# Kernel tuning notes

Hardware: AMD Instinct MI355X
Metric: run time of the kernel (lower is better)

Reference implementation:

```python
import jax, jax.numpy as jnp
import numpy as np

N, E, C, A, R = 8192, 65536, 64, 16, 8
DIMS = (1, 3, 5, 7)        # dims of l = 0..3 irrep blocks
IRDIM = sum(DIMS)          # 16
L = len(DIMS)              # 4 TP paths (0e x l -> l, 'uvu')
WN = L * C                 # conv_tp weight_numel = 256
HID = 64                   # radial MLP hidden width
AVG_NUM_NEIGH = 16.0


def setup_inputs() -> dict:
    key = jax.random.key(0)
    ks = jax.random.split(key, 18)
    f = lambda k, s: jax.random.normal(k, s, dtype=jnp.float32)
    return dict(
        node_attrs=f(ks[0], (N, A)),
        node_feats=f(ks[1], (N, C)),
        edge_attrs=f(ks[2], (E, IRDIM)),
        edge_feats=f(ks[3], (E, R)),
        edge_index=jax.random.randint(ks[4], (2, E), 0, N),
        magmom_node_inv_feats=f(ks[5], (N, R)),
        magmom_node_attrs=f(ks[6], (N, IRDIM)),
        # learned parameters (e3nn-style, no biases, 1/sqrt(fan_in) path norm)
        W_up=f(ks[7], (C, C)),
        W_r0=f(ks[8], (R + R, HID)),
        W_r1=f(ks[9], (HID, HID)),
        W_r2=f(ks[10], (HID, HID)),
        W_r3=f(ks[11], (HID, WN)),
        W_trans=f(ks[12], (WN, WN)),
        W_dens=f(ks[13], (R, 1)),
        W_lin=f(ks[14], (L, C, C)),
        W_mlin=f(ks[15], (L, C, C)),
        W_skip=f(ks[16], (L, C, A, C)),
        W_mskip=f(ks[17], (L, C, A, C)),
    )


def _per_l_linear(x, W):
    # equivariant Linear: independent channel-mixing per l block. x: [N,C,16]
    outs, o = [], 0
    for l, d in enumerate(DIMS):
        outs.append(jnp.einsum('ncm,cd->ndm', x[:, :, o:o + d], W[l]) / np.sqrt(C))
        o += d
    return jnp.concatenate(outs, axis=-1)


def _skip_tp(x, attrs, W):
    # FullyConnectedTensorProduct with scalar (0e) node attrs: (l x 0e -> l, 'uvw')
    outs, o = [], 0
    for l, d in enumerate(DIMS):
        outs.append(jnp.einsum('num,nv,uvw->nwm', x[:, :, o:o + d], attrs, W[l]) / np.sqrt(C * A))
        o += d
    return jnp.concatenate(outs, axis=-1)


def _weighted_tp(xj, attrs_e, w):
    # weighted TP of 0e node feats with lmax=3 attrs: per-edge 'uvu' weights.
    # xj: [E,C], attrs_e: [E,16], w: [E,L,C] -> [E,C,16]
    wf = jnp.repeat(w, np.array(DIMS), axis=1, total_repeat_length=IRDIM)  # [E,16,C]
    return xj[:, :, None] * attrs_e[:, None, :] * jnp.swapaxes(wf, 1, 2)


def reference(node_attrs, node_feats, edge_attrs, edge_feats, edge_index,
              magmom_node_inv_feats, magmom_node_attrs,
              W_up, W_r0, W_r1, W_r2, W_r3, W_trans, W_dens,
              W_lin, W_mlin, W_skip, W_mskip):
    sender, receiver = edge_index[0], edge_index[1]
    x = node_feats @ W_up / np.sqrt(C)                     # linear_up (0e)
    xj = x[sender]                                         # gather by sender
    h = jnp.concatenate([edge_feats, magmom_node_inv_feats[sender]], axis=-1)
    for W in (W_r0, W_r1, W_r2):                           # radial MLP (silu)
        h = jax.nn.silu(h @ W / np.sqrt(W.shape[0]))
    tp_w = (h @ W_r3 / np.sqrt(HID)).reshape(E, L, C)      # per-edge TP weights
    edge_density = jnp.tanh((edge_feats @ W_dens / np.sqrt(R)) ** 2)  # [E,1]
    mji = _weighted_tp(xj, edge_attrs, tp_w)               # [E,C,16]
    tp_w_m = (tp_w.reshape(E, WN) @ W_trans / np.sqrt(WN)).reshape(E, L, C)
    magmom_mji = _weighted_tp(xj, magmom_node_attrs[sender], tp_w_m)
    density = jax.ops.segment_sum(edge_density, receiver, num_segments=N)       # [N,1]
    message = jax.ops.segment_sum(mji, receiver, num_segments=N)                # [N,C,16]
    magmom_message = jax.ops.segment_sum(magmom_mji, receiver, num_segments=N)
    message = _per_l_linear(message, W_lin) / (density[:, :, None] + 1.0)
    message = _skip_tp(message, node_attrs, W_skip)
    magmom_message = _per_l_linear(magmom_message, W_mlin) / AVG_NUM_NEIGH
    magmom_message = _skip_tp(magmom_message, node_attrs, W_mskip)
    return message, magmom_message                         # each [N,C,16] (reshape_irreps layout)
```

## Files before the change

### kernel.cpp

```cpp
#include <hip/hip_runtime.h>

#define N_NODES 8192
#define N_EDGES 65536

typedef __attribute__((ext_vector_type(8))) short bf16x8;
typedef __attribute__((ext_vector_type(4))) float f32x4;

static __device__ __forceinline__ float bfl(unsigned v){ unsigned u=v<<16; float f; __builtin_memcpy(&f,&u,4); return f; }
static __device__ __forceinline__ float bfh(unsigned v){ unsigned u=v&0xffff0000u; float f; __builtin_memcpy(&f,&u,4); return f; }
static __device__ __forceinline__ float bfs(unsigned short h){ unsigned u=((unsigned)h)<<16; float f; __builtin_memcpy(&f,&u,4); return f; }
static __device__ __forceinline__ unsigned short f2bf(float f){ unsigned u; __builtin_memcpy(&u,&f,4); u += 0x7fffu + ((u>>16)&1u); return (unsigned short)(u>>16); }
static __device__ __forceinline__ unsigned pk(float a, float b){ return (unsigned)f2bf(a) | ((unsigned)f2bf(b)<<16); }
static __device__ __forceinline__ float silu_f(float v){ return v/(1.f+__expf(-v)); }

__global__ __launch_bounds__(256) void k_linup(const float* __restrict__ nf,
                                               const float* __restrict__ wup,
                                               float* __restrict__ x){
    __shared__ float s[4][64];
    const int t=threadIdx.x, wv=t>>6, lane=t&63;
    const int n=blockIdx.x*4+wv;
    s[wv][lane]=nf[(size_t)n*64+lane];
    __syncthreads();
    float acc=0.f;
    for(int c=0;c<64;++c) acc += s[wv][c]*wup[c*64+lane];
    x[(size_t)n*64+lane]=acc*0.125f;
}

__global__ __launch_bounds__(256) void k_wmlp(const float* __restrict__ wr0,
                                              const float* __restrict__ wr1,
                                              const float* __restrict__ wr2,
                                              unsigned short* __restrict__ w0f,
                                              unsigned short* __restrict__ w1f,
                                              unsigned short* __restrict__ w2f){
    const int b=blockIdx.x, t=threadIdx.x;
    #pragma unroll
    for(int z=0;z<2;++z){
        int idx=t*2+z;
        int lane=idx>>3, i=idx&7;
        if(b<4){
            int nt=b, k=(lane>>4)*8+i, n=nt*16+(lane&15);
            float v=(k<16)? wr0[k*64+n]*0.25f : 0.f;
            w0f[(nt*64+lane)*8+i]=f2bf(v);
        } else if(b<12){
            int q=b-4, nt=q>>1, ks=q&1;
            int k=ks*32+(lane>>4)*8+i, n=nt*16+(lane&15);
            w1f[((nt*2+ks)*64+lane)*8+i]=f2bf(wr1[k*64+n]*0.125f);
        } else {
            int q=b-12, nt=q>>1, ks=q&1;
            int k=ks*32+(lane>>4)*8+i, n=nt*16+(lane&15);
            w2f[((nt*2+ks)*64+lane)*8+i]=f2bf(wr2[k*64+n]*0.125f);
        }
    }
}

__global__ __launch_bounds__(256) void k_w3t(const float* __restrict__ wr3,
                                             const float* __restrict__ wtr,
                                             float* __restrict__ wt){
    const int k=blockIdx.x, n=threadIdx.x;
    float acc=0.f;
    for(int kk=0;kk<256;++kk) acc += wr3[k*256+kk]*wtr[kk*256+n];
    wt[k*256+n]=acc;
}

__global__ __launch_bounds__(256) void k_wtf(const float* __restrict__ wr3,
                                             const float* __restrict__ wt,
                                             unsigned short* __restrict__ wtf){
    const int b=blockIdx.x;
    const int mt=b>>1, ks=b&1, t=threadIdx.x;
    #pragma unroll
    for(int z=0;z<2;++z){
        int idx=t*2+z;
        int lane=idx>>3, i=idx&7;
        int k=ks*32+(lane>>4)*8+i;
        int n=mt*16+(lane&15);
        int j=n>>3, s=n&7;
        float v = (s<4)? wr3[k*256+s*64+j]*0.125f
                       : wt[k*256+(s-4)*64+j]*(1.f/128.f);
        wtf[((size_t)b*64+lane)*8+i]=f2bf(v);
    }
}

__global__ __launch_bounds__(256) void k_wwf(const float* __restrict__ wlin,
                                             const float* __restrict__ wmlin,
                                             const float* __restrict__ wskip,
                                             const float* __restrict__ wmskip,
                                             unsigned* __restrict__ wwf){
    const int b=blockIdx.x, ten=b>>8, lc=b&255, l=lc>>6, c=lc&63;
    const float* WL = ten? wmlin:wlin;
    const float* WS = ten? wmskip:wskip;
    const float scale = ten? (1.f/4096.f):(1.f/256.f);
    const int t=threadIdx.x, wg=t>>6, s=t&63, lane=s>>1, half=s&1;
    const int kg=lane>>4, w=wg*16+(lane&15);
    const int v0=kg*8+half*4;
    float a0=0,a1=0,a2=0,a3=0;
    for(int u=0;u<64;++u){
        float wl=WL[(l*64+c)*64+u];
        const float* wsp=&WS[(((l*64+u)*16+v0)*64)+w];
        a0+=wl*wsp[0]; a1+=wl*wsp[64]; a2+=wl*wsp[128]; a3+=wl*wsp[192];
    }
    size_t fi=(((size_t)ten*4+l)*64+c)*4+wg;
    unsigned* op=wwf + (fi*32+lane)*4 + half*2;
    op[0]=pk(a0*scale,a1*scale); op[1]=pk(a2*scale,a3*scale);
}

__global__ __launch_bounds__(256) void k_count(const int* __restrict__ recv, int* __restrict__ cnt){
    int e=blockIdx.x*256+threadIdx.x;
    atomicAdd(&cnt[recv[e]],1);
}
__global__ __launch_bounds__(1024) void k_scan(const int* __restrict__ cnt, int* __restrict__ rowptr, int* __restrict__ cur){
    __shared__ int s[1024];
    const int t=threadIdx.x;
    int c[8]; int sum=0;
    #pragma unroll
    for(int i=0;i<8;++i){ c[i]=cnt[t*8+i]; sum+=c[i]; }
    s[t]=sum; __syncthreads();
    for(int off=1;off<1024;off<<=1){
        int v=s[t]; int add=(t>=off)? s[t-off]:0;
        __syncthreads();
        s[t]=v+add;
        __syncthreads();
    }
    int run=s[t]-sum;
    #pragma unroll
    for(int i=0;i<8;++i){ rowptr[t*8+i]=run; cur[t*8+i]=run; run+=c[i]; }
    if(t==1023) rowptr[8192]=run;
}
__global__ __launch_bounds__(256) void k_scatter(const int* __restrict__ recv, int* __restrict__ cur, int* __restrict__ elist){
    int e=blockIdx.x*256+threadIdx.x;
    int r=recv[e];
    int p=atomicAdd(&cur[r],1);
    elist[p]=e;
}

__global__ __launch_bounds__(256) void k_edge2(
    const float* __restrict__ ef, const float* __restrict__ mminv,
    const int* __restrict__ sender,
    const float* __restrict__ wdens,
    const uint4* __restrict__ w0f, const uint4* __restrict__ w1f,
    const uint4* __restrict__ w2f, const uint4* __restrict__ wtf,
    const float* __restrict__ x,
    unsigned short* __restrict__ wxc, float* __restrict__ ed)
{
    __shared__ unsigned short hA[4096];
    __shared__ unsigned short hB[4096];
    __shared__ float xs[64*68];
    const int t=threadIdx.x, lane=t&63, wv=t>>6;
    const int tile=blockIdx.x*64;

    {
        const int e=t>>2, q=t&3, ge=tile+e;
        const int s=sender[ge];
        const float4* xp=(const float4*)(x+(size_t)s*64+q*16);
        float4* xw=(float4*)&xs[e*68+q*16];
        xw[0]=xp[0]; xw[1]=xp[1]; xw[2]=xp[2]; xw[3]=xp[3];
        const int se3=(e&7)<<3;
        if(q==0){
            float4 f0=*(const float4*)(ef+(size_t)ge*8);
            float4 f1=*(const float4*)(ef+(size_t)ge*8+4);
            uint4 o; o.x=pk(f0.x,f0.y); o.y=pk(f0.z,f0.w); o.z=pk(f1.x,f1.y); o.w=pk(f1.z,f1.w);
            *(uint4*)&hA[e*64 + (0^se3)]=o;
            float acc=f0.x*wdens[0]+f0.y*wdens[1]+f0.z*wdens[2]+f0.w*wdens[3]
                     +f1.x*wdens[4]+f1.y*wdens[5]+f1.z*wdens[6]+f1.w*wdens[7];
            acc*=0.35355339059327373f;
            float q2=acc*acc;
            float ex=__expf(2.f*q2);
            ed[ge]=1.f-2.f/(ex+1.f);
        } else if(q==1){
            float4 f0=*(const float4*)(mminv+(size_t)s*8);
            float4 f1=*(const float4*)(mminv+(size_t)s*8+4);
            uint4 o; o.x=pk(f0.x,f0.y); o.y=pk(f0.z,f0.w); o.z=pk(f1.x,f1.y); o.w=pk(f1.z,f1.w);
            *(uint4*)&hA[e*64 + (8^se3)]=o;
        } else if(q==2){
            *(uint4*)&hA[e*64 + (16^se3)]=make_uint4(0,0,0,0);
        } else {
            *(uint4*)&hA[e*64 + (24^se3)]=make_uint4(0,0,0,0);
        }
    }
    __syncthreads();

    const int arow=wv*16+(lane&15);
    const int akg=lane>>4;
    const int aswz=(arow&7)<<3;
    const int dcol=lane&15;
    const int drow0=wv*16+(lane>>4)*4;

    {
        uint4 av=*(const uint4*)&hA[arow*64+((akg*8)^aswz)];
        bf16x8 a; __builtin_memcpy(&a,&av,16);
        f32x4 d[4];
        #pragma unroll
        for(int nt=0;nt<4;++nt){
            uint4 bw=w0f[nt*64+lane];
            bf16x8 b; __builtin_memcpy(&b,&bw,16);
            f32x4 z={0.f,0.f,0.f,0.f};
            d[nt]=__builtin_amdgcn_mfma_f32_16x16x32_bf16(a,b,z,0,0,0);
        }
        #pragma unroll
        for(int nt=0;nt<4;++nt){
            #pragma unroll
            for(int r=0;r<4;++r){
                int e2=drow0+r, n=nt*16+dcol;
                hB[e2*64 + (n^((e2&7)<<3))]=f2bf(silu_f(d[nt][r]));
            }
        }
    }
    __syncthreads();

    {
        uint4 av0=*(const uint4*)&hB[arow*64+(((0+akg)*8)^aswz)];
        uint4 av1=*(const uint4*)&hB[arow*64+(((4+akg)*8)^aswz)];
        bf16x8 a0,a1; __builtin_memcpy(&a0,&av0,16); __builtin_memcpy(&a1,&av1,16);
        f32x4 d[4];
        #pragma unroll
        for(int nt=0;nt<4;++nt){
            uint4 bw0=w1f[(nt*2+0)*64+lane];
            uint4 bw1=w1f[(nt*2+1)*64+lane];
            bf16x8 b0,b1; __builtin_memcpy(&b0,&bw0,16); __builtin_memcpy(&b1,&bw1,16);
            f32x4 z={0.f,0.f,0.f,0.f};
            d[nt]=__builtin_amdgcn_mfma_f32_16x16x32_bf16(a0,b0,z,0,0,0);
            d[nt]=__builtin_amdgcn_mfma_f32_16x16x32_bf16(a1,b1,d[nt],0,0,0);
        }
        #pragma unroll
        for(int nt=0;nt<4;++nt){
            #pragma unroll
            for(int r=0;r<4;++r){
                int e2=drow0+r, n=nt*16+dcol;
                hA[e2*64 + (n^((e2&7)<<3))]=f2bf(silu_f(d[nt][r]));
            }
        }
    }
    __syncthreads();

    {
        uint4 av0=*(const uint4*)&hA[arow*64+(((0+akg)*8)^aswz)];
        uint4 av1=*(const uint4*)&hA[arow*64+(((4+akg)*8)^aswz)];
        bf16x8 a0,a1; __builtin_memcpy(&a0,&av0,16); __builtin_memcpy(&a1,&av1,16);
        f32x4 d[4];
        #pragma unroll
        for(int nt=0;nt<4;++nt){
            uint4 bw0=w2f[(nt*2+0)*64+lane];
            uint4 bw1=w2f[(nt*2+1)*64+lane];
            bf16x8 b0,b1; __builtin_memcpy(&b0,&bw0,16); __builtin_memcpy(&b1,&bw1,16);
            f32x4 z={0.f,0.f,0.f,0.f};
            d[nt]=__builtin_amdgcn_mfma_f32_16x16x32_bf16(a0,b0,z,0,0,0);
            d[nt]=__builtin_amdgcn_mfma_f32_16x16x32_bf16(a1,b1,d[nt],0,0,0);
        }
        #pragma unroll
        for(int nt=0;nt<4;++nt){
            #pragma unroll
            for(int r=0;r<4;++r){
                int e2=drow0+r, n=nt*16+dcol;
                hB[e2*64 + (n^((e2&7)<<3))]=f2bf(silu_f(d[nt][r]));
            }
        }
    }
    __syncthreads();

    {
        bf16x8 hb[4][2];
        #pragma unroll
        for(int nt2=0;nt2<4;++nt2){
            int erow=nt2*16+(lane&15);
            int esz=(erow&7)<<3;
            #pragma unroll
            for(int ks=0;ks<2;++ks){
                uint4 v=*(const uint4*)&hB[erow*64+(((ks*4+akg)*8)^esz)];
                __builtin_memcpy(&hb[nt2][ks],&v,16);
            }
        }
        const int g=lane>>4;
        const int jo=g>>1, sh=g&1;
        for(int mt=0;mt<8;++mt){
            int mtg=wv*8+mt;
            uint4 aw0=wtf[(mtg*2+0)*64+lane];
            uint4 aw1=wtf[(mtg*2+1)*64+lane];
            bf16x8 a0,a1; __builtin_memcpy(&a0,&aw0,16); __builtin_memcpy(&a1,&aw1,16);
            int j=mtg*2+jo;
            #pragma unroll
            for(int nt2=0;nt2<4;++nt2){
                f32x4 z={0.f,0.f,0.f,0.f};
                f32x4 d=__builtin_amdgcn_mfma_f32_16x16x32_bf16(a0,hb[nt2][0],z,0,0,0);
                d=__builtin_amdgcn_mfma_f32_16x16x32_bf16(a1,hb[nt2][1],d,0,0,0);
                int eloc=nt2*16+(lane&15);
                float xj=xs[eloc*68+j];
                uint2 o; o.x=pk(d[0]*xj,d[1]*xj); o.y=pk(d[2]*xj,d[3]*xj);
                *(uint2*)&wxc[((size_t)(tile+eloc)*64+j)*8+sh*4]=o;
            }
        }
    }
}

__global__ __launch_bounds__(256) void k_gather(
    const int* __restrict__ rowptr, const int* __restrict__ elist,
    const unsigned short* __restrict__ wxc, const float* __restrict__ ea,
    const float* __restrict__ mattr, const int* __restrict__ sender,
    const float* __restrict__ ed,
    float* __restrict__ out)
{
    const int t=threadIdx.x, wv=t>>6, lane=t&63;
    const int n=blockIdx.x*4+wv;
    const int r0=rowptr[n], r1=rowptr[n+1];
    float msg[16]; float mm[16];
    #pragma unroll
    for(int m=0;m<16;++m){ msg[m]=0.f; mm[m]=0.f; }
    float dens=0.f;
    for(int k=r0;k<r1;++k){
        int e=elist[k];
        uint4 r=*(const uint4*)(wxc+((size_t)e*64+lane)*8);
        int s=sender[e];
        float wx0=bfl(r.x),wx1=bfh(r.x),wx2=bfl(r.y),wx3=bfh(r.y);
        float wm0=bfl(r.z),wm1=bfh(r.z),wm2=bfl(r.w),wm3=bfh(r.w);
        dens+=ed[e];
        const float4* eap=(const float4*)(ea+(size_t)e*16);
        const float4* map=(const float4*)(mattr+(size_t)s*16);
        float4 A0=eap[0],A1=eap[1],A2=eap[2],A3=eap[3];
        float4 B0=map[0],B1=map[1],B2=map[2],B3=map[3];
        msg[0]+=wx0*A0.x;
        msg[1]+=wx1*A0.y;  msg[2]+=wx1*A0.z;  msg[3]+=wx1*A0.w;
        msg[4]+=wx2*A1.x;  msg[5]+=wx2*A1.y;  msg[6]+=wx2*A1.z;  msg[7]+=wx2*A1.w;  msg[8]+=wx2*A2.x;
        msg[9]+=wx3*A2.y;  msg[10]+=wx3*A2.z; msg[11]+=wx3*A2.w;
        msg[12]+=wx3*A3.x; msg[13]+=wx3*A3.y; msg[14]+=wx3*A3.z; msg[15]+=wx3*A3.w;
        mm[0]+=wm0*B0.x;
        mm[1]+=wm1*B0.y;  mm[2]+=wm1*B0.z;  mm[3]+=wm1*B0.w;
        mm[4]+=wm2*B1.x;  mm[5]+=wm2*B1.y;  mm[6]+=wm2*B1.z;  mm[7]+=wm2*B1.w;  mm[8]+=wm2*B2.x;
        mm[9]+=wm3*B2.y;  mm[10]+=wm3*B2.z; mm[11]+=wm3*B2.w;
        mm[12]+=wm3*B3.x; mm[13]+=wm3*B3.y; mm[14]+=wm3*B3.z; mm[15]+=wm3*B3.w;
    }
    float inv=1.f/(1.f+dens);
    float* mp=out+(size_t)n*1024+lane*16;
    ((float4*)mp)[0]=make_float4(msg[0]*inv,msg[1]*inv,msg[2]*inv,msg[3]*inv);
    ((float4*)mp)[1]=make_float4(msg[4]*inv,msg[5]*inv,msg[6]*inv,msg[7]*inv);
    ((float4*)mp)[2]=make_float4(msg[8]*inv,msg[9]*inv,msg[10]*inv,msg[11]*inv);
    ((float4*)mp)[3]=make_float4(msg[12]*inv,msg[13]*inv,msg[14]*inv,msg[15]*inv);
    float* qp=out+8388608+(size_t)n*1024+lane*16;
    ((float4*)qp)[0]=make_float4(mm[0],mm[1],mm[2],mm[3]);
    ((float4*)qp)[1]=make_float4(mm[4],mm[5],mm[6],mm[7]);
    ((float4*)qp)[2]=make_float4(mm[8],mm[9],mm[10],mm[11]);
    ((float4*)qp)[3]=make_float4(mm[12],mm[13],mm[14],mm[15]);
}

#define STEP0_(v0,v1,v2, cc) { \
    _Pragma("unroll") \
    for(int r_=0;r_<4;++r_){ \
        uint4 h_=*(const uint4*)&msgS[(((cc)*16+g4+r_))*8]; \
        float dr0_=v0[r_], dr1_=v1[r_], dr2_=v2[r_]; \
        acc[r_][0]+=bfl(h_.x)*dr0_; \
        acc[r_][1]+=bfh(h_.x)*dr1_; \
        acc[r_][2]+=bfl(h_.y)*dr1_; \
        acc[r_][3]+=bfh(h_.y)*dr1_; \
        acc[r_][4]+=bfl(h_.z)*dr2_; \
        acc[r_][5]+=bfh(h_.z)*dr2_; \
        acc[r_][6]+=bfl(h_.w)*dr2_; \
        acc[r_][7]+=bfh(h_.w)*dr2_; \
    } }
#define STEP1_(v0,v1, cc) { \
    _Pragma("unroll") \
    for(int r_=0;r_<4;++r_){ \
        uint4 h_=*(const uint4*)&msgS[(((cc)*16+g4+r_))*8]; \
        float dr0_=v0[r_], dr1_=v1[r_]; \
        acc[r_][0]+=bfl(h_.x)*dr0_; \
        acc[r_][1]+=bfh(h_.x)*dr1_; \
        acc[r_][2]+=bfl(h_.y)*dr1_; \
        acc[r_][3]+=bfh(h_.y)*dr1_; \
        acc[r_][4]+=bfl(h_.z)*dr1_; \
        acc[r_][5]+=bfh(h_.z)*dr1_; \
        acc[r_][6]+=bfl(h_.w)*dr1_; \
        acc[r_][7]+=bfh(h_.w)*dr1_; \
    } }
#define MFMA1_(o, b) { \
    bf16x8 f_; __builtin_memcpy(&f_,&(b),16); \
    f32x4 z_={0.f,0.f,0.f,0.f}; \
    o=__builtin_amdgcn_mfma_f32_16x16x32_bf16(afrag,f_,z_,0,0,0); }

__global__ __launch_bounds__(256) void k_final8(const float* __restrict__ attrs,
                                                const unsigned* __restrict__ wwf,
                                                float* __restrict__ out){
    __shared__ unsigned short msgS[64*16*8];
    const int blk=blockIdx.x;
    const int half=blk&1;
    const int rest=blk>>1;
    const int ten=rest>>9, nb=(rest&511)*16;
    float* base=out+(size_t)ten*8388608;
    const int t=threadIdx.x, lane=t&63, wg=t>>6;

    const float4* src=(const float4*)(base+(size_t)nb*1024);
    #pragma unroll
    for(int i=0;i<8;++i){
        int tau=i*256+t;
        int n=tau>>7, rem=tau&127, c=rem>>1, qq=rem&1;
        float4 f=src[(n<<8)+(c<<2)+half*2+qq];
        unsigned* dst=(unsigned*)&msgS[(c*16+n)*8+qq*4];
        dst[0]=pk(f.x,f.y); dst[1]=pk(f.z,f.w);
    }
    bf16x8 afrag;
    {
        int nloc=lane&15, kg=lane>>4;
        if(kg<2){
            const float* ap=attrs+(size_t)(nb+nloc)*16+kg*8;
            #pragma unroll
            for(int i=0;i<8;++i) afrag[i]=(short)f2bf(ap[i]);
        } else {
            #pragma unroll
            for(int i=0;i<8;++i) afrag[i]=0;
        }
    }
    __syncthreads();

    const int g4=(lane>>4)*4;
    float acc[4][8];
    #pragma unroll
    for(int r=0;r<4;++r)
        #pragma unroll
        for(int m=0;m<8;++m) acc[r][m]=0.f;

    const uint4* wwf4=(const uint4*)wwf;
    const int l31=lane&31;

    if(half==0){
        const uint4* p0=wwf4+((size_t)((ten*4+0)*64)*4+wg)*32+l31;
        const uint4* p1=wwf4+((size_t)((ten*4+1)*64)*4+wg)*32+l31;
        const uint4* p2=wwf4+((size_t)((ten*4+2)*64)*4+wg)*32+l31;
        uint4 A0=p0[0], A1=p1[0], A2=p2[0];
        uint4 B0=p0[128], B1=p1[128], B2=p2[128];
        f32x4 dA0,dA1,dA2, dB0,dB1,dB2;
        MFMA1_(dA0,A0); MFMA1_(dA1,A1); MFMA1_(dA2,A2);
        for(int c=0;c<64;c+=2){
            const int cA=(c+2<64)? c+2 : 63;
            const int cB=(c+3<64)? c+3 : 63;
            A0=p0[cA*128]; A1=p1[cA*128]; A2=p2[cA*128];
            MFMA1_(dB0,B0); MFMA1_(dB1,B1); MFMA1_(dB2,B2);
            STEP0_(dA0,dA1,dA2, c);
            B0=p0[cB*128]; B1=p1[cB*128]; B2=p2[cB*128];
            MFMA1_(dA0,A0); MFMA1_(dA1,A1); MFMA1_(dA2,A2);
            STEP0_(dB0,dB1,dB2, c+1);
        }
    } else {
        const uint4* p0=wwf4+((size_t)((ten*4+2)*64)*4+wg)*32+l31;
        const uint4* p1=wwf4+((size_t)((ten*4+3)*64)*4+wg)*32+l31;
        uint4 A0=p0[0], A1=p1[0];
        uint4 B0=p0[128], B1=p1[128];
        f32x4 dA0,dA1, dB0,dB1;
        MFMA1_(dA0,A0); MFMA1_(dA1,A1);
        for(int c=0;c<64;c+=2){
            const int cA=(c+2<64)? c+2 : 63;
            const int cB=(c+3<64)? c+3 : 63;
            A0=p0[cA*128]; A1=p1[cA*128];
            MFMA1_(dB0,B0); MFMA1_(dB1,B1);
            STEP1_(dA0,dA1, c);
            B0=p0[cB*128]; B1=p1[cB*128];
            MFMA1_(dA0,A0); MFMA1_(dA1,A1);
            STEP1_(dB0,dB1, c+1);
        }
    }

    const int w=wg*16+(lane&15);
    #pragma unroll
    for(int r=0;r<4;++r){
        float* op=base+(size_t)(nb+g4+r)*1024+w*16+half*8;
        ((float4*)op)[0]=make_float4(acc[r][0],acc[r][1],acc[r][2],acc[r][3]);
        ((float4*)op)[1]=make_float4(acc[r][4],acc[r][5],acc[r][6],acc[r][7]);
    }
}

extern "C" void kernel_launch(void* const* d_in, const int* in_sizes, int n_in,
                              void* d_out, int out_size, void* d_ws, size_t ws_size,
                              hipStream_t stream) {
    const float* node_attrs=(const float*)d_in[0];
    const float* node_feats=(const float*)d_in[1];
    const float* edge_attrs=(const float*)d_in[2];
    const float* edge_feats=(const float*)d_in[3];
    const int*   eidx_in  =(const int*)  d_in[4];
    const int*   sender   =eidx_in;
    const int*   recv     =eidx_in+N_EDGES;
    const float* mminv    =(const float*)d_in[5];
    const float* mattr    =(const float*)d_in[6];
    const float* wup      =(const float*)d_in[7];
    const float* wr0      =(const float*)d_in[8];
    const float* wr1      =(const float*)d_in[9];
    const float* wr2      =(const float*)d_in[10];
    const float* wr3      =(const float*)d_in[11];
    const float* wtr      =(const float*)d_in[12];
    const float* wdens    =(const float*)d_in[13];
    const float* wlin     =(const float*)d_in[14];
    const float* wmlin    =(const float*)d_in[15];
    const float* wskip    =(const float*)d_in[16];
    const float* wmskip   =(const float*)d_in[17];

    char* ws=(char*)d_ws;
    float*          x     =(float*)(ws+0);
    unsigned short* wxc   =(unsigned short*)(ws+2097152);
    float*          wt    =(float*)(ws+69206016);
    float*          ed    =(float*)(ws+73400320);
    unsigned short* wtf   =(unsigned short*)(ws+73662464);
    unsigned*       wwf   =(unsigned*)(ws+73728000);
    unsigned short* w0f   =(unsigned short*)(ws+75825152);
    unsigned short* w1f   =(unsigned short*)(ws+75829248);
    unsigned short* w2f   =(unsigned short*)(ws+75837440);
    int*            cnt   =(int*)(ws+75845632);
    int*            rowptr=(int*)(ws+75878400);
    int*            cur   =(int*)(ws+75911296);
    int*            elist =(int*)(ws+75944064);
    if(ws_size < (size_t)76206208) return;

    float* out=(float*)d_out;

    hipMemsetAsync(cnt,0,32768,stream);
    k_linup  <<<dim3(2048),dim3(256),0,stream>>>(node_feats,wup,x);
    k_wmlp   <<<dim3(20),  dim3(256),0,stream>>>(wr0,wr1,wr2,w0f,w1f,w2f);
    k_w3t    <<<dim3(64),  dim3(256),0,stream>>>(wr3,wtr,wt);
    k_wtf    <<<dim3(64),  dim3(256),0,stream>>>(wr3,wt,wtf);
    k_wwf    <<<dim3(512), dim3(256),0,stream>>>(wlin,wmlin,wskip,wmskip,wwf);
    k_count  <<<dim3(256), dim3(256),0,stream>>>(recv,cnt);
    k_scan   <<<dim3(1),   dim3(1024),0,stream>>>(cnt,rowptr,cur);
    k_scatter<<<dim3(256), dim3(256),0,stream>>>(recv,cur,elist);
    k_edge2  <<<dim3(1024),dim3(256),0,stream>>>(edge_feats,mminv,sender,wdens,
                                                 (const uint4*)w0f,(const uint4*)w1f,
                                                 (const uint4*)w2f,(const uint4*)wtf,
                                                 x,wxc,ed);
    k_gather <<<dim3(2048),dim3(256),0,stream>>>(rowptr,elist,wxc,edge_attrs,mattr,sender,ed,out);
    k_final8 <<<dim3(2048),dim3(256),0,stream>>>(node_attrs,wwf,out);
}
```

Before: 242.1 us.

## Merge preprocessing kernels into one launch and fold scatter into edge kernel

Six independent setup kernels (linear up, MLP weight packing, W3·Wtrans, weight fragment packing, combined linear/skip weights, receiver counting) are merged into a single block-indexed launch. The separate W3·Wtrans product kernel is removed and its dot products are computed inline inside the fragment packing, which drops an intermediate buffer but repeats the 256-long reduction for each element. The CSR scatter is folded into the edge MLP kernel as extra leading blocks. The goal is to cut launch count and inter-kernel gaps. The cost is heavier, divergent blocks and some redundant arithmetic.

```diff
diff --git a/kernel.cpp b/kernel.cpp
--- a/kernel.cpp
+++ b/kernel.cpp
@@ -8,105 +8,91 @@
 
 static __device__ __forceinline__ float bfl(unsigned v){ unsigned u=v<<16; float f; __builtin_memcpy(&f,&u,4); return f; }
 static __device__ __forceinline__ float bfh(unsigned v){ unsigned u=v&0xffff0000u; float f; __builtin_memcpy(&f,&u,4); return f; }
-static __device__ __forceinline__ float bfs(unsigned short h){ unsigned u=((unsigned)h)<<16; float f; __builtin_memcpy(&f,&u,4); return f; }
 static __device__ __forceinline__ unsigned short f2bf(float f){ unsigned u; __builtin_memcpy(&u,&f,4); u += 0x7fffu + ((u>>16)&1u); return (unsigned short)(u>>16); }
 static __device__ __forceinline__ unsigned pk(float a, float b){ return (unsigned)f2bf(a) | ((unsigned)f2bf(b)<<16); }
 static __device__ __forceinline__ float silu_f(float v){ return v/(1.f+__expf(-v)); }
 
-__global__ __launch_bounds__(256) void k_linup(const float* __restrict__ nf,
-                                               const float* __restrict__ wup,
-                                               float* __restrict__ x){
-    __shared__ float s[4][64];
-    const int t=threadIdx.x, wv=t>>6, lane=t&63;
-    const int n=blockIdx.x*4+wv;
-    s[wv][lane]=nf[(size_t)n*64+lane];
-    __syncthreads();
-    float acc=0.f;
-    for(int c=0;c<64;++c) acc += s[wv][c]*wup[c*64+lane];
-    x[(size_t)n*64+lane]=acc*0.125f;
+__global__ __launch_bounds__(256) void k_prep(
+    const float* __restrict__ nf,  const float* __restrict__ wup,  float* __restrict__ x,
+    const float* __restrict__ wr0, const float* __restrict__ wr1,  const float* __restrict__ wr2,
+    unsigned short* __restrict__ w0f, unsigned short* __restrict__ w1f, unsigned short* __restrict__ w2f,
+    const float* __restrict__ wr3, const float* __restrict__ wtr,  unsigned short* __restrict__ wtf,
+    const float* __restrict__ wlin, const float* __restrict__ wmlin,
+    const float* __restrict__ wskip, const float* __restrict__ wmskip, unsigned* __restrict__ wwf,
+    const int* __restrict__ recv, int* __restrict__ cnt)
+{
+    const int bid=blockIdx.x, t=threadIdx.x;
+    if(bid<2048){
+        __shared__ float s[4][64];
+        const int wv=t>>6, lane=t&63;
+        const int n=bid*4+wv;
+        s[wv][lane]=nf[(size_t)n*64+lane];
+        __syncthreads();
+        float acc=0.f;
+        for(int c=0;c<64;++c) acc += s[wv][c]*wup[c*64+lane];
+        x[(size_t)n*64+lane]=acc*0.125f;
+    } else if(bid<2068){
+        const int b=bid-2048;
+        #pragma unroll
+        for(int z=0;z<2;++z){
+            int idx=t*2+z;
+            int lane=idx>>3, i=idx&7;
+            if(b<4){
+                int nt=b, k=(lane>>4)*8+i, n=nt*16+(lane&15);
+                float v=(k<16)? wr0[k*64+n]*0.25f : 0.f;
+                w0f[(nt*64+lane)*8+i]=f2bf(v);
+            } else if(b<12){
+                int q=b-4, nt=q>>1, ks=q&1;
+                int k=ks*32+(lane>>4)*8+i, n=nt*16+(lane&15);
+                w1f[((nt*2+ks)*64+lane)*8+i]=f2bf(wr1[k*64+n]*0.125f);
+            } else {
+                int q=b-12, nt=q>>1, ks=q&1;
+                int k=ks*32+(lane>>4)*8+i, n=nt*16+(lane&15);
+                w2f[((nt*2+ks)*64+lane)*8+i]=f2bf(wr2[k*64+n]*0.125f);
+            }
+        }
+    } else if(bid<2132){
+        const int b=bid-2068;
+        const int mt=b>>1, ks=b&1;
+        #pragma unroll
+        for(int z=0;z<2;++z){
+            int idx=t*2+z;
+            int lane=idx>>3, i=idx&7;
+            int k=ks*32+(lane>>4)*8+i;
+            int n=mt*16+(lane&15);
+            int j=n>>3, s=n&7;
+            float v;
+            if(s<4) v=wr3[k*256+s*64+j]*0.125f;
+            else {
+                float acc=0.f;
+                for(int kk=0;kk<256;++kk) acc+=wr3[k*256+kk]*wtr[kk*256+(s-4)*64+j];
+                v=acc*(1.f/128.f);
+            }
+            wtf[((size_t)b*64+lane)*8+i]=f2bf(v);
+        }
+    } else if(bid<2644){
+        const int b=bid-2132, ten=b>>8, lc=b&255, l=lc>>6, c=lc&63;
+        const float* WL = ten? wmlin:wlin;
+        const float* WS = ten? wmskip:wskip;
+        const float scale = ten? (1.f/4096.f):(1.f/256.f);
+        const int wg=t>>6, s=t&63, lane=s>>1, half=s&1;
+        const int w=wg*16+(lane&15);
+        const int v0=(lane>>4)*8+half*4;
+        float a0=0,a1=0,a2=0,a3=0;
+        for(int u=0;u<64;++u){
+            float wl=WL[(l*64+c)*64+u];
+            const float* wsp=&WS[(((l*64+u)*16+v0)*64)+w];
+            a0+=wl*wsp[0]; a1+=wl*wsp[64]; a2+=wl*wsp[128]; a3+=wl*wsp[192];
+        }
+        size_t fi=(((size_t)ten*4+l)*64+c)*4+wg;
+        unsigned* op=wwf + (fi*32+lane)*4 + half*2;
+        op[0]=pk(a0*scale,a1*scale); op[1]=pk(a2*scale,a3*scale);
+    } else {
+        int e=(bid-2644)*256+t;
+        atomicAdd(&cnt[recv[e]],1);
+    }
 }
 
-__global__ __launch_bounds__(256) void k_wmlp(const float* __restrict__ wr0,
-                                              const float* __restrict__ wr1,
-                                              const float* __restrict__ wr2,
-                                              unsigned short* __restrict__ w0f,
-                                              unsigned short* __restrict__ w1f,
-                                              unsigned short* __restrict__ w2f){
-    const int b=blockIdx.x, t=threadIdx.x;
-    #pragma unroll
-    for(int z=0;z<2;++z){
-        int idx=t*2+z;
-        int lane=idx>>3, i=idx&7;
-        if(b<4){
-            int nt=b, k=(lane>>4)*8+i, n=nt*16+(lane&15);
-            float v=(k<16)? wr0[k*64+n]*0.25f : 0.f;
-            w0f[(nt*64+lane)*8+i]=f2bf(v);
-        } else if(b<12){
-            int q=b-4, nt=q>>1, ks=q&1;
-            int k=ks*32+(lane>>4)*8+i, n=nt*16+(lane&15);
-            w1f[((nt*2+ks)*64+lane)*8+i]=f2bf(wr1[k*64+n]*0.125f);
-        } else {
-            int q=b-12, nt=q>>1, ks=q&1;
-            int k=ks*32+(lane>>4)*8+i, n=nt*16+(lane&15);
-            w2f[((nt*2+ks)*64+lane)*8+i]=f2bf(wr2[k*64+n]*0.125f);
-        }
-    }
-}
-
-__global__ __launch_bounds__(256) void k_w3t(const float* __restrict__ wr3,
-                                             const float* __restrict__ wtr,
-                                             float* __restrict__ wt){
-    const int k=blockIdx.x, n=threadIdx.x;
-    float acc=0.f;
-    for(int kk=0;kk<256;++kk) acc += wr3[k*256+kk]*wtr[kk*256+n];
-    wt[k*256+n]=acc;
-}
-
-__global__ __launch_bounds__(256) void k_wtf(const float* __restrict__ wr3,
-                                             const float* __restrict__ wt,
-                                             unsigned short* __restrict__ wtf){
-    const int b=blockIdx.x;
-    const int mt=b>>1, ks=b&1, t=threadIdx.x;
-    #pragma unroll
-    for(int z=0;z<2;++z){
-        int idx=t*2+z;
-        int lane=idx>>3, i=idx&7;
-        int k=ks*32+(lane>>4)*8+i;
-        int n=mt*16+(lane&15);
-        int j=n>>3, s=n&7;
-        float v = (s<4)? wr3[k*256+s*64+j]*0.125f
-                       : wt[k*256+(s-4)*64+j]*(1.f/128.f);
-        wtf[((size_t)b*64+lane)*8+i]=f2bf(v);
-    }
-}
-
-__global__ __launch_bounds__(256) void k_wwf(const float* __restrict__ wlin,
-                                             const float* __restrict__ wmlin,
-                                             const float* __restrict__ wskip,
-                                             const float* __restrict__ wmskip,
-                                             unsigned* __restrict__ wwf){
-    const int b=blockIdx.x, ten=b>>8, lc=b&255, l=lc>>6, c=lc&63;
-    const float* WL = ten? wmlin:wlin;
-    const float* WS = ten? wmskip:wskip;
-    const float scale = ten? (1.f/4096.f):(1.f/256.f);
-    const int t=threadIdx.x, wg=t>>6, s=t&63, lane=s>>1, half=s&1;
-    const int kg=lane>>4, w=wg*16+(lane&15);
-    const int v0=kg*8+half*4;
-    float a0=0,a1=0,a2=0,a3=0;
-    for(int u=0;u<64;++u){
-        float wl=WL[(l*64+c)*64+u];
-        const float* wsp=&WS[(((l*64+u)*16+v0)*64)+w];
-        a0+=wl*wsp[0]; a1+=wl*wsp[64]; a2+=wl*wsp[128]; a3+=wl*wsp[192];
-    }
-    size_t fi=(((size_t)ten*4+l)*64+c)*4+wg;
-    unsigned* op=wwf + (fi*32+lane)*4 + half*2;
-    op[0]=pk(a0*scale,a1*scale); op[1]=pk(a2*scale,a3*scale);
-}
-
-__global__ __launch_bounds__(256) void k_count(const int* __restrict__ recv, int* __restrict__ cnt){
-    int e=blockIdx.x*256+threadIdx.x;
-    atomicAdd(&cnt[recv[e]],1);
-}
 __global__ __launch_bounds__(1024) void k_scan(const int* __restrict__ cnt, int* __restrict__ rowptr, int* __restrict__ cur){
     __shared__ int s[1024];
     const int t=threadIdx.x;
@@ -125,14 +111,9 @@
     for(int i=0;i<8;++i){ rowptr[t*8+i]=run; cur[t*8+i]=run; run+=c[i]; }
     if(t==1023) rowptr[8192]=run;
 }
-__global__ __launch_bounds__(256) void k_scatter(const int* __restrict__ recv, int* __restrict__ cur, int* __restrict__ elist){
-    int e=blockIdx.x*256+threadIdx.x;
-    int r=recv[e];
-    int p=atomicAdd(&cur[r],1);
-    elist[p]=e;
-}
-
-__global__ __launch_bounds__(256) void k_edge2(
+
+__global__ __launch_bounds__(256) void k_mid(
+    const int* __restrict__ recv, int* __restrict__ cur, int* __restrict__ elist,
     const float* __restrict__ ef, const float* __restrict__ mminv,
     const int* __restrict__ sender,
     const float* __restrict__ wdens,
@@ -144,8 +125,16 @@
     __shared__ unsigned short hA[4096];
     __shared__ unsigned short hB[4096];
     __shared__ float xs[64*68];
-    const int t=threadIdx.x, lane=t&63, wv=t>>6;
-    const int tile=blockIdx.x*64;
+    const int bid=blockIdx.x, t=threadIdx.x;
+    if(bid<256){
+        int e=bid*256+t;
+        int r=recv[e];
+        int p=atomicAdd(&cur[r],1);
+        elist[p]=e;
+        return;
+    }
+    const int lane=t&63, wv=t>>6;
+    const int tile=(bid-256)*64;
 
     {
         const int e=t>>2, q=t&3, ge=tile+e;
@@ -489,7 +478,6 @@
     char* ws=(char*)d_ws;
     float*          x     =(float*)(ws+0);
     unsigned short* wxc   =(unsigned short*)(ws+2097152);
-    float*          wt    =(float*)(ws+69206016);
     float*          ed    =(float*)(ws+73400320);
     unsigned short* wtf   =(unsigned short*)(ws+73662464);
     unsigned*       wwf   =(unsigned*)(ws+73728000);
@@ -505,15 +493,14 @@
     float* out=(float*)d_out;
 
     hipMemsetAsync(cnt,0,32768,stream);
-    k_linup  <<<dim3(2048),dim3(256),0,stream>>>(node_feats,wup,x);
-    k_wmlp   <<<dim3(20),  dim3(256),0,stream>>>(wr0,wr1,wr2,w0f,w1f,w2f);
-    k_w3t    <<<dim3(64),  dim3(256),0,stream>>>(wr3,wtr,wt);
-    k_wtf    <<<dim3(64),  dim3(256),0,stream>>>(wr3,wt,wtf);
-    k_wwf    <<<dim3(512), dim3(256),0,stream>>>(wlin,wmlin,wskip,wmskip,wwf);
-    k_count  <<<dim3(256), dim3(256),0,stream>>>(recv,cnt);
+    k_prep   <<<dim3(2900),dim3(256),0,stream>>>(node_feats,wup,x,
+                                                 wr0,wr1,wr2,w0f,w1f,w2f,
+                                                 wr3,wtr,wtf,
+                                                 wlin,wmlin,wskip,wmskip,wwf,
+                                                 recv,cnt);
     k_scan   <<<dim3(1),   dim3(1024),0,stream>>>(cnt,rowptr,cur);
-    k_scatter<<<dim3(256), dim3(256),0,stream>>>(recv,cur,elist);
-    k_edge2  <<<dim3(1024),dim3(256),0,stream>>>(edge_feats,mminv,sender,wdens,
+    k_mid    <<<dim3(1280),dim3(256),0,stream>>>(recv,cur,elist,
+                                                 edge_feats,mminv,sender,wdens,
                                                  (const uint4*)w0f,(const uint4*)w1f,
                                                  (const uint4*)w2f,(const uint4*)wtf,
                                                  x,wxc,ed);
```

Result: faster. 231.8 us (-4.3%).
